# Kernel tuning notes

Measured on AMD Instinct MI355X. Metric: run time of the kernel, lower is better.

The kernel has to match this reference:

```python
import jax, jax.numpy as jnp
import numpy as np

N, E, F_IN, G = 100000, 1600000, 128, 64
H1, H2, H3 = 64, 32, 16


def _xavier(key, fan_in, fan_out):
    lim = np.sqrt(6.0 / (fan_in + fan_out))
    return jax.random.uniform(key, (fan_in, fan_out), jnp.float32, -lim, lim)


def setup_inputs() -> dict:
    key = jax.random.key(0)
    ks = jax.random.split(key, 16)
    x = jax.random.normal(ks[0], (N, F_IN), jnp.float32)
    edge_index = jax.random.randint(ks[1], (2, E), 0, N, dtype=jnp.int32)
    batch = jnp.sort(jax.random.randint(ks[2], (N,), 0, G, dtype=jnp.int32))
    d = {
        "x": x,
        "W1": _xavier(ks[3], F_IN, H1), "b1": jnp.zeros((H1,), jnp.float32),
        "W2": _xavier(ks[4], H1, H2), "b2": jnp.zeros((H2,), jnp.float32),
        "W3": _xavier(ks[5], H2, H3), "b3": jnp.zeros((H3,), jnp.float32),
        "g1": jnp.ones((H1,), jnp.float32), "be1": jnp.zeros((H1,), jnp.float32),
        "g2": jnp.ones((H2,), jnp.float32), "be2": jnp.zeros((H2,), jnp.float32),
        "g3": jnp.ones((H3,), jnp.float32), "be3": jnp.zeros((H3,), jnp.float32),
        "attn_w": _xavier(ks[6], 3 * H3, 3), "attn_b": jnp.zeros((3,), jnp.float32),
        "fc1_w": _xavier(ks[7], H3, H3), "fc1_b": jnp.zeros((H3,), jnp.float32),
        "fc2_w": _xavier(ks[8], H3, H3 // 2), "fc2_b": jnp.zeros((H3 // 2,), jnp.float32),
        "out_w": _xavier(ks[9], H3 // 2, 1), "out_b": jnp.zeros((1,), jnp.float32),
        "edge_index": edge_index,
        "batch": batch,
        "num_graphs": G,
    }
    return d


def _lrelu(z):
    return jnp.where(z > 0, z, 0.1 * z)


def _bn(h, gamma, beta, eps=1e-5):
    # BatchNorm1d forward with batch statistics (biased variance), as torch training-mode math
    m = jnp.mean(h, axis=0)
    v = jnp.mean(jnp.square(h - m), axis=0)
    return (h - m) * jax.lax.rsqrt(v + eps) * gamma + beta


def reference(x, W1, b1, W2, b2, W3, b3, g1, be1, g2, be2, g3, be3,
              attn_w, attn_b, fc1_w, fc1_b, fc2_w, fc2_b, out_w, out_b,
              edge_index, batch, num_graphs):
    src, dst = edge_index[0], edge_index[1]
    n = x.shape[0]
    # GCN degree with self-loops: deg[i] = 1 + #incoming edges
    deg = jax.ops.segment_sum(jnp.ones((src.shape[0],), x.dtype), dst, num_segments=n) + 1.0
    dis = jax.lax.rsqrt(deg)                      # deg^-1/2, [N]
    enorm = dis[src] * dis[dst]                   # per-edge norm, [E]
    selfw = dis * dis                             # self-loop norm, [N]

    def gcn(h, W, b):
        hw = h @ W                                # [N, H]
        agg = jax.ops.segment_sum(hw[src] * enorm[:, None], dst, num_segments=n)
        return agg + selfw[:, None] * hw + b

    x1 = _lrelu(_bn(gcn(x, W1, b1), g1, be1))     # dropout = identity (eval)
    x2 = _lrelu(_bn(gcn(x1, W2, b2), g2, be2))    # residual skipped: 64 != 32
    x3 = _lrelu(_bn(gcn(x2, W3, b3), g3, be3))    # residual skipped: 32 != 16

    # multi-pool over graphs
    ones_n = jnp.ones((n,), x.dtype)
    counts = jax.ops.segment_sum(ones_n, batch, num_segments=num_graphs)  # [G]
    x_sum = jax.ops.segment_sum(x3, batch, num_segments=num_graphs)       # [G, H3]
    x_mean = x_sum / jnp.maximum(counts, 1.0)[:, None]
    x_max = jax.ops.segment_max(x3, batch, num_segments=num_graphs)

    pooled = jnp.concatenate([x_mean, x_max, x_sum], axis=1)              # [G, 3*H3]
    aw = jax.nn.softmax(pooled @ attn_w + attn_b, axis=1)                 # [G, 3]
    xg = aw[:, 0:1] * x_mean + aw[:, 1:2] * x_max + aw[:, 2:3] * x_sum    # [G, H3]

    xg = _lrelu(xg @ fc1_w + fc1_b)
    xg = _lrelu(xg @ fc2_w + fc2_b)
    out = jax.nn.sigmoid(xg @ out_w + out_b)                              # [G, 1]
    return out
```

## Files before the change

### kernel.cpp

```cpp
#include <hip/hip_runtime.h>

#define GG 64
#define SREP 32
#define BSH 14
typedef unsigned long long ull;
typedef unsigned short u16;
typedef unsigned int uint;

__device__ __forceinline__ u16 f2b(float x) {
    unsigned u = __float_as_uint(x);
    return (u16)((u + 0x7FFFu + ((u >> 16) & 1u)) >> 16);
}

__device__ __forceinline__ void add8(const uint4 q, float* acc) {
    acc[0] += __uint_as_float(q.x << 16);
    acc[1] += __uint_as_float(q.x & 0xFFFF0000u);
    acc[2] += __uint_as_float(q.y << 16);
    acc[3] += __uint_as_float(q.y & 0xFFFF0000u);
    acc[4] += __uint_as_float(q.z << 16);
    acc[5] += __uint_as_float(q.z & 0xFFFF0000u);
    acc[6] += __uint_as_float(q.w << 16);
    acc[7] += __uint_as_float(q.w & 0xFFFF0000u);
}

__global__ __launch_bounds__(256) void k_hist(const int* __restrict__ src,
                                              const int* __restrict__ dst,
                                              int* __restrict__ cnt4, int E, int n) {
    const int part = blockIdx.x & 7;
    const int nblk = gridDim.x >> 3;
    const int bser = blockIdx.x >> 3;
    const int lo = (int)(((long long)part * n) >> 3);
    const int hi = (part == 7) ? n : (int)(((long long)(part + 1) * n) >> 3);
    for (int e = bser * 256 + threadIdx.x; e < E; e += nblk * 256) {
        int d = dst[e];
        if (d >= lo && d < hi) {
            int b = min(src[e] >> BSH, 7);
            atomicAdd(&cnt4[(d << 3) + b], 1);
        }
    }
}

__global__ void k_scanA(const int* __restrict__ cnt4, int* __restrict__ rp,
                        int* __restrict__ bsum, float* __restrict__ dis, int n) {
    __shared__ int s[256];
    int i = blockIdx.x * 256 + threadIdx.x;
    int v = 0;
    if (i < n) {
        #pragma unroll
        for (int b = 0; b < 8; ++b) v += cnt4[(i << 3) + b];
        dis[i] = rsqrtf((float)v + 1.0f);
    }
    s[threadIdx.x] = v;
    __syncthreads();
    for (int off = 1; off < 256; off <<= 1) {
        int t = (threadIdx.x >= off) ? s[threadIdx.x - off] : 0;
        __syncthreads();
        s[threadIdx.x] += t;
        __syncthreads();
    }
    if (i < n) rp[i] = s[threadIdx.x] - v;
    if (threadIdx.x == 255) bsum[blockIdx.x] = s[255];
}

__global__ void k_scanB(int* __restrict__ bsum, int nb) {
    __shared__ int s[512];
    int v = (threadIdx.x < nb) ? bsum[threadIdx.x] : 0;
    s[threadIdx.x] = v;
    __syncthreads();
    for (int off = 1; off < 512; off <<= 1) {
        int t = (threadIdx.x >= off) ? s[threadIdx.x - off] : 0;
        __syncthreads();
        s[threadIdx.x] += t;
        __syncthreads();
    }
    if (threadIdx.x < nb) bsum[threadIdx.x] = s[threadIdx.x] - v;
}

__global__ void k_scanC(int* __restrict__ rp, const int* __restrict__ bsum,
                        const int* __restrict__ cnt4, int* __restrict__ cursor4,
                        int n, int E) {
    int i = blockIdx.x * 256 + threadIdx.x;
    if (i < n) {
        int r = rp[i] + bsum[blockIdx.x];
        rp[i] = r;
        int run = r;
        #pragma unroll
        for (int b = 0; b < 8; ++b) {
            cursor4[(i << 3) + b] = run;
            run += cnt4[(i << 3) + b];
        }
    }
    if (i == 0) rp[n] = E;
}

__global__ __launch_bounds__(256) void k_scatter(const int* __restrict__ src,
                                                 const int* __restrict__ dst,
                                                 int* __restrict__ cursor4,
                                                 uint* __restrict__ epack, int E, int n) {
    const int part = blockIdx.x & 7;
    const int nblk = gridDim.x >> 3;
    const int bser = blockIdx.x >> 3;
    const int lo = (int)(((long long)part * n) >> 3);
    const int hi = (part == 7) ? n : (int)(((long long)(part + 1) * n) >> 3);
    for (int e = bser * 256 + threadIdx.x; e < E; e += nblk * 256) {
        int d = dst[e];
        if (d >= lo && d < hi) {
            int s = src[e];
            int b = min(s >> BSH, 7);
            int pos = atomicAdd(&cursor4[(d << 3) + b], 1);
            epack[pos] = (uint)s;
        }
    }
}

template <int FIN, int FOUT, bool BN>
__global__ __launch_bounds__(256) void k_mm(const float* __restrict__ h,
                                            const float* __restrict__ W,
                                            const float* __restrict__ dis,
                                            const float* __restrict__ stats,
                                            const float* __restrict__ gma,
                                            const float* __restrict__ bta,
                                            u16* __restrict__ hw, int n) {
    constexpr int FX  = FOUT / 4;
    constexpr int TY  = 256 / FX;
    constexpr int NT  = TY * 4;
    constexpr int LDA = FIN + ((FOUT == 64) ? 2 : 1);
    __shared__ float sA[NT * LDA];
    __shared__ float sW[FIN * FOUT];
    __shared__ float sSc[FIN], sSh[FIN];

    if (BN && threadIdx.x < FIN) {
        int f = threadIdx.x;
        float s = 0.f, q = 0.f;
        #pragma unroll 8
        for (int r = 0; r < SREP; ++r) {
            s += stats[(r << 7) + f];
            q += stats[(r << 7) + 64 + f];
        }
        float inv_n = 1.0f / (float)n;
        float m = s * inv_n;
        float var = fmaxf(q * inv_n - m * m, 0.f);
        float sc = rsqrtf(var + 1e-5f) * gma[f];
        sSc[f] = sc;
        sSh[f] = bta[f] - m * sc;
    }
    for (int i = threadIdx.x; i < FIN * FOUT / 4; i += 256)
        ((float4*)sW)[i] = ((const float4*)W)[i];
    if (BN) __syncthreads();

    const int node0 = blockIdx.x * NT;
    constexpr int LD4 = NT * FIN / 4 / 256;
    #pragma unroll
    for (int i = 0; i < LD4; ++i) {
        int idx4 = i * 256 + threadIdx.x;
        int row = idx4 / (FIN / 4);
        int c4  = idx4 % (FIN / 4);
        int gn  = node0 + row;
        float4 v = make_float4(0.f, 0.f, 0.f, 0.f);
        if (gn < n) v = ((const float4*)(h + (long long)gn * FIN))[c4];
        if (BN) {
            int f = c4 * 4;
            float t;
            t = fmaf(v.x, sSc[f + 0], sSh[f + 0]); v.x = t > 0.f ? t : 0.1f * t;
            t = fmaf(v.y, sSc[f + 1], sSh[f + 1]); v.y = t > 0.f ? t : 0.1f * t;
            t = fmaf(v.z, sSc[f + 2], sSh[f + 2]); v.z = t > 0.f ? t : 0.1f * t;
            t = fmaf(v.w, sSc[f + 3], sSh[f + 3]); v.w = t > 0.f ? t : 0.1f * t;
        }
        float* p = &sA[row * LDA + c4 * 4];
        p[0] = v.x; p[1] = v.y; p[2] = v.z; p[3] = v.w;
    }
    __syncthreads();

    const int tx = threadIdx.x % FX;
    const int ty = threadIdx.x / FX;
    float acc[4][4];
    #pragma unroll
    for (int i = 0; i < 4; ++i)
        #pragma unroll
        for (int j = 0; j < 4; ++j) acc[i][j] = 0.f;

    #pragma unroll 8
    for (int k = 0; k < FIN; ++k) {
        float4 wv = *((const float4*)&sW[k * FOUT + tx * 4]);
        float a0 = sA[(ty * 4 + 0) * LDA + k];
        float a1 = sA[(ty * 4 + 1) * LDA + k];
        float a2 = sA[(ty * 4 + 2) * LDA + k];
        float a3 = sA[(ty * 4 + 3) * LDA + k];
        acc[0][0] = fmaf(a0, wv.x, acc[0][0]); acc[0][1] = fmaf(a0, wv.y, acc[0][1]);
        acc[0][2] = fmaf(a0, wv.z, acc[0][2]); acc[0][3] = fmaf(a0, wv.w, acc[0][3]);
        acc[1][0] = fmaf(a1, wv.x, acc[1][0]); acc[1][1] = fmaf(a1, wv.y, acc[1][1]);
        acc[1][2] = fmaf(a1, wv.z, acc[1][2]); acc[1][3] = fmaf(a1, wv.w, acc[1][3]);
        acc[2][0] = fmaf(a2, wv.x, acc[2][0]); acc[2][1] = fmaf(a2, wv.y, acc[2][1]);
        acc[2][2] = fmaf(a2, wv.z, acc[2][2]); acc[2][3] = fmaf(a2, wv.w, acc[2][3]);
        acc[3][0] = fmaf(a3, wv.x, acc[3][0]); acc[3][1] = fmaf(a3, wv.y, acc[3][1]);
        acc[3][2] = fmaf(a3, wv.z, acc[3][2]); acc[3][3] = fmaf(a3, wv.w, acc[3][3]);
    }

    #pragma unroll
    for (int i = 0; i < 4; ++i) {
        int gn = node0 + ty * 4 + i;
        if (gn < n) {
            float dv = dis[gn];
            ushort4 o;
            o.x = f2b(acc[i][0] * dv); o.y = f2b(acc[i][1] * dv);
            o.z = f2b(acc[i][2] * dv); o.w = f2b(acc[i][3] * dv);
            ((ushort4*)(hw + (long long)gn * FOUT))[tx] = o;
        }
    }
}

template <int FOUT, int T>
__global__ __launch_bounds__(256) void k_aggt(const u16* __restrict__ hwb,
                                              const uint* __restrict__ epack,
                                              const int* __restrict__ rp,
                                              const int* __restrict__ cursor4,
                                              const float* __restrict__ dis,
                                              const float* __restrict__ bias,
                                              float* __restrict__ y,
                                              float* __restrict__ stats,
                                              int n, int nbuck) {
    constexpr int LPN = FOUT / 8;
    constexpr int GPB = 256 / LPN;
    constexpr int NPB = GPB * T;
    constexpr int RS  = FOUT / 8;
    __shared__ float ssum[FOUT], ssq[FOUT];
    for (int i = threadIdx.x; i < FOUT; i += 256) { ssum[i] = 0.f; ssq[i] = 0.f; }
    __syncthreads();
    const int grp = threadIdx.x / LPN;
    const int fq  = threadIdx.x % LPN;
    const uint4* hw4 = (const uint4*)hwb;

    int nd[T], jp[T];
    float acc[T][8];
    #pragma unroll
    for (int t = 0; t < T; ++t) {
        nd[t] = blockIdx.x * NPB + grp * T + t;
        jp[t] = (nd[t] < n) ? rp[nd[t]] : 0;
        #pragma unroll
        for (int i = 0; i < 8; ++i) acc[t][i] = 0.f;
    }

    for (int b = 0; b < nbuck; ++b) {
        int je[T];
        #pragma unroll
        for (int t = 0; t < T; ++t)
            je[t] = (nd[t] < n) ? cursor4[(nd[t] << 3) + b] : 0;
        bool more = (jp[0] < je[0]);
        #pragma unroll
        for (int t = 1; t < T; ++t) more |= (jp[t] < je[t]);
        while (more) {
            more = false;
            uint idx[T];
            bool act[T];
            #pragma unroll
            for (int t = 0; t < T; ++t) {
                act[t] = jp[t] < je[t];
                idx[t] = epack[act[t] ? jp[t] : 0];
            }
            uint4 q[T];
            #pragma unroll
            for (int t = 0; t < T; ++t) {
                int row = act[t] ? (int)idx[t] : min(nd[t], n - 1);
                q[t] = hw4[(long long)row * RS + fq];
            }
            #pragma unroll
            for (int t = 0; t < T; ++t) {
                if (act[t]) {
                    add8(q[t], acc[t]);
                    ++jp[t];
                    more |= (jp[t] < je[t]);
                }
            }
        }
    }

    float lsum[8] = {0,0,0,0,0,0,0,0}, lsq[8] = {0,0,0,0,0,0,0,0};
    float b8[8];
    #pragma unroll
    for (int i = 0; i < 8; ++i) b8[i] = bias[fq * 8 + i];
    #pragma unroll
    for (int t = 0; t < T; ++t) {
        int node = nd[t];
        if (node < n) {
            uint4 qs = hw4[(long long)node * RS + fq];
            add8(qs, acc[t]);
            float dv = dis[node];
            #pragma unroll
            for (int i = 0; i < 8; ++i) acc[t][i] = fmaf(dv, acc[t][i], b8[i]);
            float4* y4 = (float4*)y;
            long long o = (long long)node * (FOUT / 4) + fq * 2;
            y4[o]     = make_float4(acc[t][0], acc[t][1], acc[t][2], acc[t][3]);
            y4[o + 1] = make_float4(acc[t][4], acc[t][5], acc[t][6], acc[t][7]);
            #pragma unroll
            for (int i = 0; i < 8; ++i) {
                lsum[i] += acc[t][i];
                lsq[i] = fmaf(acc[t][i], acc[t][i], lsq[i]);
            }
        }
    }
    #pragma unroll
    for (int i = 0; i < 8; ++i) {
        atomicAdd(&ssum[fq * 8 + i], lsum[i]);
        atomicAdd(&ssq[fq * 8 + i], lsq[i]);
    }
    __syncthreads();
    float* st = stats + ((blockIdx.x & (SREP - 1)) << 7);
    for (int i = threadIdx.x; i < FOUT; i += 256) {
        atomicAdd(&st[i], ssum[i]);
        atomicAdd(&st[64 + i], ssq[i]);
    }
}

template <int FOUT>
__global__ __launch_bounds__(256) void k_agg(const u16* __restrict__ hwb,
                                             const uint* __restrict__ epack,
                                             const int* __restrict__ rp,
                                             const float* __restrict__ dis,
                                             const float* __restrict__ bias,
                                             float* __restrict__ y,
                                             float* __restrict__ stats, int n) {
    constexpr int LPN = FOUT / 8;
    constexpr int NPB = 256 / LPN;
    constexpr int RS  = FOUT / 8;
    __shared__ float ssum[FOUT], ssq[FOUT];
    for (int i = threadIdx.x; i < FOUT; i += 256) { ssum[i] = 0.f; ssq[i] = 0.f; }
    __syncthreads();
    const int local = threadIdx.x / LPN;
    const int fq = threadIdx.x % LPN;
    const uint4* hw4 = (const uint4*)hwb;
    float b8[8];
    #pragma unroll
    for (int i = 0; i < 8; ++i) b8[i] = bias[fq * 8 + i];
    float lsum[8] = {0,0,0,0,0,0,0,0}, lsq[8] = {0,0,0,0,0,0,0,0};

    int node = blockIdx.x * NPB + local;
    if (node < n) {
        int j0 = rp[node], j1 = rp[node + 1];
        float acc[8] = {0,0,0,0,0,0,0,0};
        int j = j0;
        for (; j + 8 <= j1; j += 8) {
            uint s0 = epack[j + 0], s1 = epack[j + 1], s2 = epack[j + 2], s3 = epack[j + 3];
            uint s4 = epack[j + 4], s5 = epack[j + 5], s6 = epack[j + 6], s7 = epack[j + 7];
            uint4 q0 = hw4[(long long)s0 * RS + fq];
            uint4 q1 = hw4[(long long)s1 * RS + fq];
            uint4 q2 = hw4[(long long)s2 * RS + fq];
            uint4 q3 = hw4[(long long)s3 * RS + fq];
            uint4 q4 = hw4[(long long)s4 * RS + fq];
            uint4 q5 = hw4[(long long)s5 * RS + fq];
            uint4 q6 = hw4[(long long)s6 * RS + fq];
            uint4 q7 = hw4[(long long)s7 * RS + fq];
            add8(q0, acc); add8(q1, acc); add8(q2, acc); add8(q3, acc);
            add8(q4, acc); add8(q5, acc); add8(q6, acc); add8(q7, acc);
        }
        for (; j + 2 <= j1; j += 2) {
            uint s0 = epack[j + 0], s1 = epack[j + 1];
            uint4 q0 = hw4[(long long)s0 * RS + fq];
            uint4 q1 = hw4[(long long)s1 * RS + fq];
            add8(q0, acc); add8(q1, acc);
        }
        for (; j < j1; ++j) {
            uint4 q = hw4[(long long)epack[j] * RS + fq];
            add8(q, acc);
        }
        uint4 qs = hw4[(long long)node * RS + fq];
        add8(qs, acc);
        float dv = dis[node];
        #pragma unroll
        for (int i = 0; i < 8; ++i) acc[i] = fmaf(dv, acc[i], b8[i]);
        float4* y4 = (float4*)y;
        long long o = (long long)node * (FOUT / 4) + fq * 2;
        y4[o]     = make_float4(acc[0], acc[1], acc[2], acc[3]);
        y4[o + 1] = make_float4(acc[4], acc[5], acc[6], acc[7]);
        #pragma unroll
        for (int i = 0; i < 8; ++i) {
            lsum[i] += acc[i];
            lsq[i] = fmaf(acc[i], acc[i], lsq[i]);
        }
    }
    #pragma unroll
    for (int i = 0; i < 8; ++i) {
        atomicAdd(&ssum[fq * 8 + i], lsum[i]);
        atomicAdd(&ssq[fq * 8 + i], lsq[i]);
    }
    __syncthreads();
    float* st = stats + ((blockIdx.x & (SREP - 1)) << 7);
    for (int i = threadIdx.x; i < FOUT; i += 256) {
        atomicAdd(&st[i], ssum[i]);
        atomicAdd(&st[64 + i], ssq[i]);
    }
}

__global__ void k_pool_graph(const float* __restrict__ yraw, const int* __restrict__ batch,
                             const float* __restrict__ stats, const float* __restrict__ gma,
                             const float* __restrict__ bta, int n,
                             float* __restrict__ psum, float* __restrict__ pmax,
                             float* __restrict__ pcnt) {
    const int g    = blockIdx.x >> 3;
    const int part = blockIdx.x & 7;
    const int f = threadIdx.x & 15;
    float s = 0.f, q = 0.f;
    #pragma unroll 8
    for (int r = 0; r < SREP; ++r) {
        s += stats[(r << 7) + f];
        q += stats[(r << 7) + 64 + f];
    }
    float inv_n = 1.0f / (float)n;
    float m = s * inv_n;
    float var = fmaxf(q * inv_n - m * m, 0.f);
    float sc = rsqrtf(var + 1e-5f) * gma[f];
    float sh = bta[f] - m * sc;

    __shared__ int s_lo, s_hi;
    if (threadIdx.x == 0) {
        int lo = 0, hi = n;
        while (lo < hi) { int mid = (lo + hi) >> 1; if (batch[mid] < g) lo = mid + 1; else hi = mid; }
        s_lo = lo;
        hi = n;
        while (lo < hi) { int mid = (lo + hi) >> 1; if (batch[mid] < g + 1) lo = mid + 1; else hi = mid; }
        s_hi = lo;
    }
    __syncthreads();
    const int gs = s_lo, len = s_hi - s_lo;
    const int start = gs + (int)(((long long)len * part) >> 3);
    const int end   = gs + (int)(((long long)len * (part + 1)) >> 3);
    float lsum = 0.f, lmax = -3.0e38f;
    for (long long idx = (long long)start * 16 + threadIdx.x; idx < (long long)end * 16; idx += blockDim.x) {
        float t = fmaf(yraw[idx], sc, sh);
        float v = t > 0.f ? t : 0.1f * t;
        lsum += v;
        lmax = fmaxf(lmax, v);
    }
    __shared__ float ss[256], sm[256];
    ss[threadIdx.x] = lsum; sm[threadIdx.x] = lmax;
    __syncthreads();
    for (int off = 128; off >= 16; off >>= 1) {
        if (threadIdx.x < off) {
            ss[threadIdx.x] += ss[threadIdx.x + off];
            sm[threadIdx.x] = fmaxf(sm[threadIdx.x], sm[threadIdx.x + off]);
        }
        __syncthreads();
    }
    if (threadIdx.x < 16) {
        psum[(((g << 3) + part) << 4) + threadIdx.x] = ss[threadIdx.x];
        pmax[(((g << 3) + part) << 4) + threadIdx.x] = sm[threadIdx.x];
    }
    if (threadIdx.x == 0) pcnt[(g << 3) + part] = (float)(end - start);
}

__global__ void k_head(const float* __restrict__ psum, const float* __restrict__ pmax,
                       const float* __restrict__ pcnt,
                       const float* __restrict__ attn_w, const float* __restrict__ attn_b,
                       const float* __restrict__ fc1_w, const float* __restrict__ fc1_b,
                       const float* __restrict__ fc2_w, const float* __restrict__ fc2_b,
                       const float* __restrict__ out_w, const float* __restrict__ out_b,
                       float* __restrict__ out) {
    int g = threadIdx.x;
    if (g >= GG) return;
    float xs[16], xm[16], xx[16];
    float c = 0.f;
    for (int p = 0; p < 8; ++p) c += pcnt[(g << 3) + p];
    c = fmaxf(c, 1.0f);
    for (int f = 0; f < 16; ++f) { xs[f] = 0.f; xx[f] = -3.0e38f; }
    for (int p = 0; p < 8; ++p) {
        for (int f = 0; f < 16; ++f) {
            xs[f] += psum[(((g << 3) + p) << 4) + f];
            xx[f] = fmaxf(xx[f], pmax[(((g << 3) + p) << 4) + f]);
        }
    }
    for (int f = 0; f < 16; ++f) xm[f] = xs[f] / c;
    float lg[3];
    for (int cI = 0; cI < 3; ++cI) {
        float a = attn_b[cI];
        for (int f = 0; f < 16; ++f) {
            a += xm[f] * attn_w[f * 3 + cI];
            a += xx[f] * attn_w[(16 + f) * 3 + cI];
            a += xs[f] * attn_w[(32 + f) * 3 + cI];
        }
        lg[cI] = a;
    }
    float mx = fmaxf(lg[0], fmaxf(lg[1], lg[2]));
    float e0 = expf(lg[0] - mx), e1 = expf(lg[1] - mx), e2 = expf(lg[2] - mx);
    float inv = 1.0f / (e0 + e1 + e2);
    float a0 = e0 * inv, a1 = e1 * inv, a2 = e2 * inv;
    float xg[16];
    for (int f = 0; f < 16; ++f) xg[f] = a0 * xm[f] + a1 * xx[f] + a2 * xs[f];
    float t1[16];
    for (int j = 0; j < 16; ++j) {
        float a = fc1_b[j];
        for (int k = 0; k < 16; ++k) a += xg[k] * fc1_w[k * 16 + j];
        t1[j] = a > 0.f ? a : 0.1f * a;
    }
    float t2[8];
    for (int j = 0; j < 8; ++j) {
        float a = fc2_b[j];
        for (int k = 0; k < 16; ++k) a += t1[k] * fc2_w[k * 8 + j];
        t2[j] = a > 0.f ? a : 0.1f * a;
    }
    float o = out_b[0];
    for (int k = 0; k < 8; ++k) o += t2[k] * out_w[k];
    o = 1.0f / (1.0f + expf(-o));
    out[g] = o;
}

extern "C" void kernel_launch(void* const* d_in, const int* in_sizes, int n_in,
                              void* d_out, int out_size, void* d_ws, size_t ws_size,
                              hipStream_t stream) {
    const float* x      = (const float*)d_in[0];
    const float* W1     = (const float*)d_in[1];  const float* b1   = (const float*)d_in[2];
    const float* W2     = (const float*)d_in[3];  const float* b2   = (const float*)d_in[4];
    const float* W3     = (const float*)d_in[5];  const float* b3   = (const float*)d_in[6];
    const float* g1     = (const float*)d_in[7];  const float* be1  = (const float*)d_in[8];
    const float* g2     = (const float*)d_in[9];  const float* be2  = (const float*)d_in[10];
    const float* g3     = (const float*)d_in[11]; const float* be3  = (const float*)d_in[12];
    const float* attn_w = (const float*)d_in[13]; const float* attn_b = (const float*)d_in[14];
    const float* fc1_w  = (const float*)d_in[15]; const float* fc1_b  = (const float*)d_in[16];
    const float* fc2_w  = (const float*)d_in[17]; const float* fc2_b  = (const float*)d_in[18];
    const float* out_w  = (const float*)d_in[19]; const float* out_b  = (const float*)d_in[20];
    const int* edge_index = (const int*)d_in[21];
    const int* batch      = (const int*)d_in[22];

    const int N = in_sizes[0] / 128;
    const int E = in_sizes[21] / 2;
    const int* srcp = edge_index;
    const int* dstp = edge_index + E;
    const int nb = (N + 255) / 256;
    const int NBUCK = min((N + (1 << BSH) - 1) >> BSH, 8);

    char* ws = (char*)d_ws;
    float* dis    = (float*)(ws);
    int*   rp     = (int*)(ws + 0x100000);
    int*   bsum   = (int*)(ws + 0x180000);
    float* stats1 = (float*)(ws + 0x180800);
    float* stats2 = (float*)(ws + 0x184800);
    float* stats3 = (float*)(ws + 0x188800);
    float* psum   = (float*)(ws + 0x80000);
    float* pmax   = psum + GG * 8 * 16;
    float* pcnt   = pmax + GG * 8 * 16;
    int*   cnt4    = (int*)(ws + 0x190000);
    int*   cursor4 = cnt4 + (size_t)8 * N;
    uint*  epack   = (uint*)(cursor4 + (size_t)8 * N);
    float* buf1    = (float*)((char*)epack + (((size_t)E * 4 + 255) & ~(size_t)255));
    u16*   hwb     = (u16*)(buf1 + (size_t)N * 64);

    hipMemsetAsync(cnt4, 0, (size_t)N * 32, stream);
    k_hist<<<2048, 256, 0, stream>>>(srcp, dstp, cnt4, E, N);
    k_scanA<<<nb, 256, 0, stream>>>(cnt4, rp, bsum, dis, N);
    k_scanB<<<1, 512, 0, stream>>>(bsum, nb);
    k_scanC<<<nb, 256, 0, stream>>>(rp, bsum, cnt4, cursor4, N, E);
    k_scatter<<<2048, 256, 0, stream>>>(srcp, dstp, cursor4, epack, E, N);
    hipMemsetAsync(stats1, 0, 3 * SREP * 512, stream);

    k_mm<128, 64, false><<<(N + 63) / 64, 256, 0, stream>>>(
        x, W1, dis, nullptr, nullptr, nullptr, hwb, N);
    k_aggt<64, 4><<<(N + 127) / 128, 256, 0, stream>>>(
        hwb, epack, rp, cursor4, dis, b1, buf1, stats1, N, NBUCK);

    k_mm<64, 32, true><<<(N + 127) / 128, 256, 0, stream>>>(
        buf1, W2, dis, stats1, g1, be1, hwb, N);
    k_aggt<32, 4><<<(N + 255) / 256, 256, 0, stream>>>(
        hwb, epack, rp, cursor4, dis, b2, buf1, stats2, N, NBUCK);

    k_mm<32, 16, true><<<(N + 255) / 256, 256, 0, stream>>>(
        buf1, W3, dis, stats2, g2, be2, hwb, N);
    k_agg<16><<<(N + 127) / 128, 256, 0, stream>>>(hwb, epack, rp, dis, b3, buf1, stats3, N);

    k_pool_graph<<<GG * 8, 256, 0, stream>>>(buf1, batch, stats3, g3, be3, N, psum, pmax, pcnt);
    k_head<<<1, 64, 0, stream>>>(psum, pmax, pcnt, attn_w, attn_b,
                                 fc1_w, fc1_b, fc2_w, fc2_b, out_w, out_b,
                                 (float*)d_out);
}
```

Baseline: 521.7 us.

## Fuse edge scatter and first-layer GEMM into one heterogeneous kernel launch

Merges the CSR scatter kernel and the layer-1 x@W1 matmul into one grid, where the first 2048 blocks do the atomic edge scatter and the rest compute the dense projection. The goal is to run the latency-bound scatter alongside the compute- and bandwidth-bound GEMM and to drop one launch. The GEMM blocks now read x straight from global memory per thread rather than staging tiles in LDS. Every block also reserves 32KB of shared memory, including the scatter blocks, which could limit how many blocks fit per CU.

```diff
diff --git a/kernel.cpp b/kernel.cpp
--- a/kernel.cpp
+++ b/kernel.cpp
@@ -93,22 +93,81 @@
     if (i == 0) rp[n] = E;
 }
 
-__global__ __launch_bounds__(256) void k_scatter(const int* __restrict__ src,
+__global__ __launch_bounds__(256) void k_scat_mm(const int* __restrict__ src,
                                                  const int* __restrict__ dst,
                                                  int* __restrict__ cursor4,
-                                                 uint* __restrict__ epack, int E, int n) {
-    const int part = blockIdx.x & 7;
-    const int nblk = gridDim.x >> 3;
-    const int bser = blockIdx.x >> 3;
-    const int lo = (int)(((long long)part * n) >> 3);
-    const int hi = (part == 7) ? n : (int)(((long long)(part + 1) * n) >> 3);
-    for (int e = bser * 256 + threadIdx.x; e < E; e += nblk * 256) {
-        int d = dst[e];
-        if (d >= lo && d < hi) {
-            int s = src[e];
-            int b = min(s >> BSH, 7);
-            int pos = atomicAdd(&cursor4[(d << 3) + b], 1);
-            epack[pos] = (uint)s;
+                                                 uint* __restrict__ epack, int E, int n,
+                                                 const float* __restrict__ x,
+                                                 const float* __restrict__ W1,
+                                                 const float* __restrict__ dis,
+                                                 u16* __restrict__ hw) {
+    __shared__ float sW[128 * 64];
+    if (blockIdx.x < 2048) {
+        const int part = blockIdx.x & 7;
+        const int nblk = 2048 >> 3;
+        const int bser = blockIdx.x >> 3;
+        const int lo = (int)(((long long)part * n) >> 3);
+        const int hi = (part == 7) ? n : (int)(((long long)(part + 1) * n) >> 3);
+        for (int e = bser * 256 + threadIdx.x; e < E; e += nblk * 256) {
+            int d = dst[e];
+            if (d >= lo && d < hi) {
+                int s = src[e];
+                int b = min(s >> BSH, 7);
+                int pos = atomicAdd(&cursor4[(d << 3) + b], 1);
+                epack[pos] = (uint)s;
+            }
+        }
+    } else {
+        for (int i = threadIdx.x; i < 128 * 64 / 4; i += 256)
+            ((float4*)sW)[i] = ((const float4*)W1)[i];
+        __syncthreads();
+        const int tx = threadIdx.x & 15;
+        const int ty = threadIdx.x >> 4;
+        const int node0 = (int)(blockIdx.x - 2048) * 64;
+        const float* xr[4];
+        #pragma unroll
+        for (int i = 0; i < 4; ++i) {
+            int gn = node0 + ty * 4 + i;
+            xr[i] = x + (long long)min(gn, n - 1) * 128;
+        }
+        float acc[4][4];
+        #pragma unroll
+        for (int i = 0; i < 4; ++i)
+            #pragma unroll
+            for (int j = 0; j < 4; ++j) acc[i][j] = 0.f;
+
+        for (int k0 = 0; k0 < 128; k0 += 4) {
+            float4 av[4];
+            #pragma unroll
+            for (int i = 0; i < 4; ++i)
+                av[i] = *((const float4*)&xr[i][k0]);
+            #pragma unroll
+            for (int kk = 0; kk < 4; ++kk) {
+                float4 wv = *((const float4*)&sW[(k0 + kk) * 64 + tx * 4]);
+                float a0 = (&av[0].x)[kk];
+                float a1 = (&av[1].x)[kk];
+                float a2 = (&av[2].x)[kk];
+                float a3 = (&av[3].x)[kk];
+                acc[0][0] = fmaf(a0, wv.x, acc[0][0]); acc[0][1] = fmaf(a0, wv.y, acc[0][1]);
+                acc[0][2] = fmaf(a0, wv.z, acc[0][2]); acc[0][3] = fmaf(a0, wv.w, acc[0][3]);
+                acc[1][0] = fmaf(a1, wv.x, acc[1][0]); acc[1][1] = fmaf(a1, wv.y, acc[1][1]);
+                acc[1][2] = fmaf(a1, wv.z, acc[1][2]); acc[1][3] = fmaf(a1, wv.w, acc[1][3]);
+                acc[2][0] = fmaf(a2, wv.x, acc[2][0]); acc[2][1] = fmaf(a2, wv.y, acc[2][1]);
+                acc[2][2] = fmaf(a2, wv.z, acc[2][2]); acc[2][3] = fmaf(a2, wv.w, acc[2][3]);
+                acc[3][0] = fmaf(a3, wv.x, acc[3][0]); acc[3][1] = fmaf(a3, wv.y, acc[3][1]);
+                acc[3][2] = fmaf(a3, wv.z, acc[3][2]); acc[3][3] = fmaf(a3, wv.w, acc[3][3]);
+            }
+        }
+        #pragma unroll
+        for (int i = 0; i < 4; ++i) {
+            int gn = node0 + ty * 4 + i;
+            if (gn < n) {
+                float dv = dis[gn];
+                ushort4 o;
+                o.x = f2b(acc[i][0] * dv); o.y = f2b(acc[i][1] * dv);
+                o.z = f2b(acc[i][2] * dv); o.w = f2b(acc[i][3] * dv);
+                ((ushort4*)(hw + (long long)gn * 64))[tx] = o;
+            }
         }
     }
 }
@@ -547,11 +606,10 @@
     k_scanA<<<nb, 256, 0, stream>>>(cnt4, rp, bsum, dis, N);
     k_scanB<<<1, 512, 0, stream>>>(bsum, nb);
     k_scanC<<<nb, 256, 0, stream>>>(rp, bsum, cnt4, cursor4, N, E);
-    k_scatter<<<2048, 256, 0, stream>>>(srcp, dstp, cursor4, epack, E, N);
     hipMemsetAsync(stats1, 0, 3 * SREP * 512, stream);
 
-    k_mm<128, 64, false><<<(N + 63) / 64, 256, 0, stream>>>(
-        x, W1, dis, nullptr, nullptr, nullptr, hwb, N);
+    k_scat_mm<<<2048 + (N + 63) / 64, 256, 0, stream>>>(
+        srcp, dstp, cursor4, epack, E, N, x, W1, dis, hwb);
     k_aggt<64, 4><<<(N + 127) / 128, 256, 0, stream>>>(
         hwb, epack, rp, cursor4, dis, b1, buf1, stats1, N, NBUCK);
 
```

Measured after the change: 512.3 us (median of 2 runs). No clear change (-1.8%).
